# Performance work log

Hardware: AMD Instinct MI355X
Metric: run time of the kernel (lower is better)

Reference implementation:

```python
import jax, jax.numpy as jnp
import numpy as np

NUM_FIELDS = 50
CARD = 10000  # per-field cardinality; global index = x + field_offset
FACTOR_DIM = 64
ATT_SIZE = 64
BATCH = 2048


def setup_inputs() -> dict:
    key = jax.random.key(0)
    ks = jax.random.split(key, 5)
    x = jax.random.randint(ks[0], (BATCH, NUM_FIELDS), 0, CARD, dtype=jnp.int64)
    emb = jax.random.normal(ks[1], (NUM_FIELDS * CARD, FACTOR_DIM), jnp.float32) * 0.1
    W1 = jax.random.normal(ks[2], (FACTOR_DIM, ATT_SIZE), jnp.float32) * 0.1
    b1 = jnp.zeros((ATT_SIZE,), jnp.float32)
    w2 = jax.random.normal(ks[3], (ATT_SIZE, 1), jnp.float32) * 0.1
    b2 = jnp.zeros((1,), jnp.float32)
    lin_w = jax.random.normal(ks[4], (NUM_FIELDS * CARD, 1), jnp.float32) * 0.1
    lin_b = jnp.zeros((1,), jnp.float32)
    return {"x": x, "emb": emb, "W1": W1, "b1": b1, "w2": w2, "b2": b2,
            "lin_w": lin_w, "lin_b": lin_b}


def reference(x, emb, W1, b1, w2, b2, lin_w, lin_b):
    F = NUM_FIELDS
    offsets = (jnp.arange(F, dtype=x.dtype) * CARD)[None, :]  # [1, F]
    idx = x + offsets                                          # [B, F] global ids
    factors = emb[idx]                                         # [B, F, D]
    iu, ju = np.triu_indices(F, k=1)                           # P = F*(F-1)/2 pairs (i < j)
    inter = factors[:, iu, :] * factors[:, ju, :]              # [B, P, D]
    # attention MLP: Dense -> ReLU -> Dense(1) -> Softmax over pair axis
    h = jax.nn.relu(jnp.einsum('bpd,da->bpa', inter, W1) + b1)
    logits = jnp.einsum('bpa,ao->bpo', h, w2) + b2             # [B, P, 1]
    scores = jax.nn.softmax(logits, axis=1)
    inter_sum = jnp.sum(inter, axis=-1, keepdims=True)         # [B, P, 1]
    attended = jnp.sum(inter_sum * scores, axis=1)             # [B, 1]
    linear = jnp.sum(lin_w[idx], axis=1) + lin_b               # [B, 1]
    return linear + attended
```

## Files before the change

kernel.cpp:

```cpp
#include <hip/hip_runtime.h>
#include <hip/hip_bf16.h>

#define NF 50
#define NFP 52
#define NG 13
#define NCARD 10000
#define FD 64
#define NB 2
#define FROW 72
#define FBAT (NFP * FROW)

typedef _Float16 h16x8 __attribute__((ext_vector_type(8)));
typedef float f32x4 __attribute__((ext_vector_type(4)));

__global__ __launch_bounds__(256, 4) void afm_main(
    const int* __restrict__ x,
    const float* __restrict__ emb,
    const float* __restrict__ W1,
    const float* __restrict__ b1,
    const float* __restrict__ w2,
    const float* __restrict__ lin_w,
    const float* __restrict__ lin_b,
    float* __restrict__ out)
{
    __shared__ __align__(16) _Float16 fach[NB * FBAT];
    __shared__ float cmb[4][3];

    const int b0   = blockIdx.x * NB;
    const int tid  = threadIdx.x;
    const int lane = tid & 63;
    const int wid  = tid >> 6;
    const int n16  = lane & 15;
    const int quad = lane >> 4;

    for (int t = tid; t < NB * NFP * 8; t += 256) {
        int rowid = t >> 3, q = t & 7;
        int bb = (rowid >= NFP) ? 1 : 0;
        int f = rowid - bb * NFP;
        h16x8 h = {0, 0, 0, 0, 0, 0, 0, 0};
        if (f < NF) {
            int gid = x[(b0 + bb) * NF + f] + f * NCARD;
            const float* src = emb + (size_t)gid * FD + q * 8;
            float4 v0 = *(const float4*)(src);
            float4 v1 = *(const float4*)(src + 4);
            h[0] = (_Float16)v0.x; h[1] = (_Float16)v0.y;
            h[2] = (_Float16)v0.z; h[3] = (_Float16)v0.w;
            h[4] = (_Float16)v1.x; h[5] = (_Float16)v1.y;
            h[6] = (_Float16)v1.z; h[7] = (_Float16)v1.w;
        }
        *(h16x8*)(fach + (size_t)rowid * FROW + q * 8) = h;
    }

    h16x8 afragW[8];
    #pragma unroll
    for (int mt = 0; mt < 4; ++mt) {
        #pragma unroll
        for (int ks = 0; ks < 2; ++ks) {
            h16x8 v;
            #pragma unroll
            for (int jj = 0; jj < 8; ++jj)
                v[jj] = (_Float16)W1[(ks * 32 + quad * 8 + jj) * 64 + mt * 16 + n16];
            afragW[mt * 2 + ks] = v;
        }
    }
    h16x8 aones = {(_Float16)1, (_Float16)1, (_Float16)1, (_Float16)1,
                   (_Float16)1, (_Float16)1, (_Float16)1, (_Float16)1};
    f32x4 b1v[4], w2v[4];
    #pragma unroll
    for (int mt = 0; mt < 4; ++mt) {
        const float4 bb = *(const float4*)(b1 + mt * 16 + quad * 4);
        const float4 ww = *(const float4*)(w2 + mt * 16 + quad * 4);
        b1v[mt] = (f32x4){bb.x, bb.y, bb.z, bb.w};
        w2v[mt] = (f32x4){ww.x, ww.y, ww.z, ww.w};
    }
    __syncthreads();

    const int mybatch = wid >> 1;
    const _Float16* fb = fach + mybatch * FBAT;
    const int a4 = n16 >> 2, b4 = n16 & 3;
    const int gi_lo = (wid & 1) ? 4 : 0;
    const int gi_hi = (wid & 1) ? NG : 4;

    float m = -1e30f, se = 0.f, sei = 0.f;

    for (int gi = gi_lo; gi < gi_hi; ++gi) {
        const int i = gi * 4 + a4;
        const _Float16* ri = fb + (size_t)i * FROW + quad * 8;
        const h16x8 ri0 = *(const h16x8*)(ri);
        const h16x8 ri1 = *(const h16x8*)(ri + 32);
        for (int gj = gi; gj < NG; ++gj) {
            const int j = gj * 4 + b4;
            const _Float16* rj = fb + (size_t)j * FROW + quad * 8;
            h16x8 pr0 = ri0 * (*(const h16x8*)(rj));
            h16x8 pr1 = ri1 * (*(const h16x8*)(rj + 32));

            f32x4 accS = __builtin_amdgcn_mfma_f32_16x16x32_f16(aones, pr0, (f32x4){0.f, 0.f, 0.f, 0.f}, 0, 0, 0);
            accS = __builtin_amdgcn_mfma_f32_16x16x32_f16(aones, pr1, accS, 0, 0, 0);

            float lacc = 0.f;
            #pragma unroll
            for (int mt = 0; mt < 4; ++mt) {
                f32x4 acc = __builtin_amdgcn_mfma_f32_16x16x32_f16(afragW[mt * 2 + 0], pr0, b1v[mt], 0, 0, 0);
                acc = __builtin_amdgcn_mfma_f32_16x16x32_f16(afragW[mt * 2 + 1], pr1, acc, 0, 0, 0);
                #pragma unroll
                for (int r = 0; r < 4; ++r)
                    lacc += fmaxf(acc[r], 0.f) * w2v[mt][r];
            }
            lacc += __shfl_xor(lacc, 16, 64);
            lacc += __shfl_xor(lacc, 32, 64);

            const bool valid = (i < j) && (j < NF);
            float nm = fmaxf(m, valid ? lacc : -1e30f);
            float sc = __expf(m - nm);
            float e  = valid ? __expf(lacc - nm) : 0.f;
            se  = se * sc + e;
            sei = sei * sc + e * accS[0];
            m = nm;
        }
    }

    #pragma unroll
    for (int d = 1; d <= 8; d <<= 1) {
        float m2   = __shfl_xor(m, d, 64);
        float se2  = __shfl_xor(se, d, 64);
        float sei2 = __shfl_xor(sei, d, 64);
        float nm = fmaxf(m, m2);
        float a = __expf(m - nm), bsc = __expf(m2 - nm);
        se  = se * a + se2 * bsc;
        sei = sei * a + sei2 * bsc;
        m = nm;
    }

    float lin = 0.f;
    if ((wid & 1) == 0) {
        if (lane < NF) {
            int gid = x[(b0 + mybatch) * NF + lane] + lane * NCARD;
            lin = lin_w[gid];
        }
        #pragma unroll
        for (int d = 1; d <= 32; d <<= 1) lin += __shfl_xor(lin, d, 64);
    }

    if (lane == 0) { cmb[wid][0] = m; cmb[wid][1] = se; cmb[wid][2] = sei; }
    __syncthreads();
    if ((wid & 1) == 0 && lane == 0) {
        float m2 = cmb[wid + 1][0], se2 = cmb[wid + 1][1], sei2 = cmb[wid + 1][2];
        float nm = fmaxf(m, m2);
        float a = __expf(m - nm), bsc = __expf(m2 - nm);
        float tse  = se * a + se2 * bsc;
        float tsei = sei * a + sei2 * bsc;
        out[b0 + mybatch] = lin + lin_b[0] + tsei / tse;
    }
}

extern "C" void kernel_launch(void* const* d_in, const int* in_sizes, int n_in,
                              void* d_out, int out_size, void* d_ws, size_t ws_size,
                              hipStream_t stream) {
    const int*   x     = (const int*)d_in[0];
    const float* emb   = (const float*)d_in[1];
    const float* W1    = (const float*)d_in[2];
    const float* b1    = (const float*)d_in[3];
    const float* w2    = (const float*)d_in[4];
    const float* lin_w = (const float*)d_in[6];
    const float* lin_b = (const float*)d_in[7];
    float* out = (float*)d_out;
    const int batch = out_size;
    afm_main<<<batch / NB, 256, 0, stream>>>(x, emb, W1, b1, w2, lin_w, lin_b, out);
}
```

Measured before the change: 217.2 us.

## One batch row per block, pre-pack W1 fragments, drop online-softmax max tracking

```diff
diff --git a/kernel.cpp b/kernel.cpp
--- a/kernel.cpp
+++ b/kernel.cpp
@@ -6,40 +6,53 @@
 #define NG 13
 #define NCARD 10000
 #define FD 64
-#define NB 2
 #define FROW 72
-#define FBAT (NFP * FROW)
 
 typedef _Float16 h16x8 __attribute__((ext_vector_type(8)));
 typedef float f32x4 __attribute__((ext_vector_type(4)));
 
+__global__ void afm_pre(const float* __restrict__ W1, _Float16* __restrict__ w1f) {
+    const int slot = blockIdx.x * 4 + (threadIdx.x >> 6);
+    const int lane = threadIdx.x & 63;
+    const int n16 = lane & 15, quad = lane >> 4;
+    const int mt = slot >> 1, ks = slot & 1;
+    h16x8 v;
+    #pragma unroll
+    for (int jj = 0; jj < 8; ++jj)
+        v[jj] = (_Float16)W1[(ks * 32 + quad * 8 + jj) * 64 + mt * 16 + n16];
+    *(h16x8*)(w1f + ((size_t)(slot * 64 + lane)) * 8) = v;
+}
+
 __global__ __launch_bounds__(256, 4) void afm_main(
     const int* __restrict__ x,
     const float* __restrict__ emb,
-    const float* __restrict__ W1,
     const float* __restrict__ b1,
     const float* __restrict__ w2,
     const float* __restrict__ lin_w,
     const float* __restrict__ lin_b,
+    const _Float16* __restrict__ w1f,
     float* __restrict__ out)
 {
-    __shared__ __align__(16) _Float16 fach[NB * FBAT];
-    __shared__ float cmb[4][3];
+    __shared__ __align__(16) _Float16 fach[NFP * FROW];
+    __shared__ float cmb[4][2];
+    __shared__ float s_lin;
 
-    const int b0   = blockIdx.x * NB;
+    const int b    = blockIdx.x;
     const int tid  = threadIdx.x;
     const int lane = tid & 63;
     const int wid  = tid >> 6;
     const int n16  = lane & 15;
     const int quad = lane >> 4;
 
-    for (int t = tid; t < NB * NFP * 8; t += 256) {
-        int rowid = t >> 3, q = t & 7;
-        int bb = (rowid >= NFP) ? 1 : 0;
-        int f = rowid - bb * NFP;
+    float linv = 0.f;
+    if (wid == 3 && lane < NF)
+        linv = lin_w[x[b * NF + lane] + lane * NCARD];
+
+    for (int t = tid; t < NFP * 8; t += 256) {
+        int f = t >> 3, q = t & 7;
         h16x8 h = {0, 0, 0, 0, 0, 0, 0, 0};
         if (f < NF) {
-            int gid = x[(b0 + bb) * NF + f] + f * NCARD;
+            int gid = x[b * NF + f] + f * NCARD;
             const float* src = emb + (size_t)gid * FD + q * 8;
             float4 v0 = *(const float4*)(src);
             float4 v1 = *(const float4*)(src + 4);
@@ -48,21 +61,13 @@
             h[4] = (_Float16)v1.x; h[5] = (_Float16)v1.y;
             h[6] = (_Float16)v1.z; h[7] = (_Float16)v1.w;
         }
-        *(h16x8*)(fach + (size_t)rowid * FROW + q * 8) = h;
+        *(h16x8*)(fach + (size_t)f * FROW + q * 8) = h;
     }
 
     h16x8 afragW[8];
     #pragma unroll
-    for (int mt = 0; mt < 4; ++mt) {
-        #pragma unroll
-        for (int ks = 0; ks < 2; ++ks) {
-            h16x8 v;
-            #pragma unroll
-            for (int jj = 0; jj < 8; ++jj)
-                v[jj] = (_Float16)W1[(ks * 32 + quad * 8 + jj) * 64 + mt * 16 + n16];
-            afragW[mt * 2 + ks] = v;
-        }
-    }
+    for (int s = 0; s < 8; ++s)
+        afragW[s] = *(const h16x8*)(w1f + ((size_t)(s * 64 + lane)) * 8);
     h16x8 aones = {(_Float16)1, (_Float16)1, (_Float16)1, (_Float16)1,
                    (_Float16)1, (_Float16)1, (_Float16)1, (_Float16)1};
     f32x4 b1v[4], w2v[4];
@@ -75,81 +80,69 @@
     }
     __syncthreads();
 
-    const int mybatch = wid >> 1;
-    const _Float16* fb = fach + mybatch * FBAT;
     const int a4 = n16 >> 2, b4 = n16 & 3;
-    const int gi_lo = (wid & 1) ? 4 : 0;
-    const int gi_hi = (wid & 1) ? NG : 4;
+    float se = 0.f, sei = 0.f;
 
-    float m = -1e30f, se = 0.f, sei = 0.f;
-
-    for (int gi = gi_lo; gi < gi_hi; ++gi) {
+    for (int gi = wid; gi < NG; gi += 4) {
         const int i = gi * 4 + a4;
-        const _Float16* ri = fb + (size_t)i * FROW + quad * 8;
+        const _Float16* ri = fach + (size_t)i * FROW + quad * 8;
         const h16x8 ri0 = *(const h16x8*)(ri);
         const h16x8 ri1 = *(const h16x8*)(ri + 32);
+
+        const _Float16* rjp = fach + (size_t)(gi * 4 + b4) * FROW + quad * 8;
+        h16x8 nj0 = *(const h16x8*)(rjp);
+        h16x8 nj1 = *(const h16x8*)(rjp + 32);
+
         for (int gj = gi; gj < NG; ++gj) {
-            const int j = gj * 4 + b4;
-            const _Float16* rj = fb + (size_t)j * FROW + quad * 8;
-            h16x8 pr0 = ri0 * (*(const h16x8*)(rj));
-            h16x8 pr1 = ri1 * (*(const h16x8*)(rj + 32));
+            h16x8 rj0 = nj0, rj1 = nj1;
+            if (gj + 1 < NG) {
+                rjp += 4 * FROW;
+                nj0 = *(const h16x8*)(rjp);
+                nj1 = *(const h16x8*)(rjp + 32);
+            }
+            h16x8 pr0 = ri0 * rj0;
+            h16x8 pr1 = ri1 * rj1;
 
             f32x4 accS = __builtin_amdgcn_mfma_f32_16x16x32_f16(aones, pr0, (f32x4){0.f, 0.f, 0.f, 0.f}, 0, 0, 0);
             accS = __builtin_amdgcn_mfma_f32_16x16x32_f16(aones, pr1, accS, 0, 0, 0);
 
-            float lacc = 0.f;
+            float lp[4];
             #pragma unroll
             for (int mt = 0; mt < 4; ++mt) {
                 f32x4 acc = __builtin_amdgcn_mfma_f32_16x16x32_f16(afragW[mt * 2 + 0], pr0, b1v[mt], 0, 0, 0);
                 acc = __builtin_amdgcn_mfma_f32_16x16x32_f16(afragW[mt * 2 + 1], pr1, acc, 0, 0, 0);
-                #pragma unroll
-                for (int r = 0; r < 4; ++r)
-                    lacc += fmaxf(acc[r], 0.f) * w2v[mt][r];
+                float s0 = fmaxf(acc[0], 0.f) * w2v[mt][0] + fmaxf(acc[1], 0.f) * w2v[mt][1];
+                float s1 = fmaxf(acc[2], 0.f) * w2v[mt][2] + fmaxf(acc[3], 0.f) * w2v[mt][3];
+                lp[mt] = s0 + s1;
             }
+            float lacc = (lp[0] + lp[1]) + (lp[2] + lp[3]);
             lacc += __shfl_xor(lacc, 16, 64);
             lacc += __shfl_xor(lacc, 32, 64);
 
+            const int j = gj * 4 + b4;
             const bool valid = (i < j) && (j < NF);
-            float nm = fmaxf(m, valid ? lacc : -1e30f);
-            float sc = __expf(m - nm);
-            float e  = valid ? __expf(lacc - nm) : 0.f;
-            se  = se * sc + e;
-            sei = sei * sc + e * accS[0];
-            m = nm;
+            float e = valid ? __expf(lacc) : 0.f;
+            se  += e;
+            sei += e * accS[0];
         }
     }
 
     #pragma unroll
     for (int d = 1; d <= 8; d <<= 1) {
-        float m2   = __shfl_xor(m, d, 64);
-        float se2  = __shfl_xor(se, d, 64);
-        float sei2 = __shfl_xor(sei, d, 64);
-        float nm = fmaxf(m, m2);
-        float a = __expf(m - nm), bsc = __expf(m2 - nm);
-        se  = se * a + se2 * bsc;
-        sei = sei * a + sei2 * bsc;
-        m = nm;
+        se  += __shfl_xor(se, d, 64);
+        sei += __shfl_xor(sei, d, 64);
     }
-
-    float lin = 0.f;
-    if ((wid & 1) == 0) {
-        if (lane < NF) {
-            int gid = x[(b0 + mybatch) * NF + lane] + lane * NCARD;
-            lin = lin_w[gid];
-        }
+    if (wid == 3) {
         #pragma unroll
-        for (int d = 1; d <= 32; d <<= 1) lin += __shfl_xor(lin, d, 64);
+        for (int d = 1; d <= 32; d <<= 1) linv += __shfl_xor(linv, d, 64);
+        if (lane == 0) s_lin = linv;
     }
-
-    if (lane == 0) { cmb[wid][0] = m; cmb[wid][1] = se; cmb[wid][2] = sei; }
+    if (lane == 0) { cmb[wid][0] = se; cmb[wid][1] = sei; }
     __syncthreads();
-    if ((wid & 1) == 0 && lane == 0) {
-        float m2 = cmb[wid + 1][0], se2 = cmb[wid + 1][1], sei2 = cmb[wid + 1][2];
-        float nm = fmaxf(m, m2);
-        float a = __expf(m - nm), bsc = __expf(m2 - nm);
-        float tse  = se * a + se2 * bsc;
-        float tsei = sei * a + sei2 * bsc;
-        out[b0 + mybatch] = lin + lin_b[0] + tsei / tse;
+    if (tid == 0) {
+        float tse  = (cmb[0][0] + cmb[1][0]) + (cmb[2][0] + cmb[3][0]);
+        float tsei = (cmb[0][1] + cmb[1][1]) + (cmb[2][1] + cmb[3][1]);
+        out[b] = s_lin + lin_b[0] + tsei / tse;
     }
 }
 
@@ -164,6 +157,9 @@
     const float* lin_w = (const float*)d_in[6];
     const float* lin_b = (const float*)d_in[7];
     float* out = (float*)d_out;
+
+    _Float16* w1f = (_Float16*)d_ws;
+    afm_pre<<<2, 256, 0, stream>>>(W1, w1f);
     const int batch = out_size;
-    afm_main<<<batch / NB, 256, 0, stream>>>(x, emb, W1, b1, w2, lin_w, lin_b, out);
+    afm_main<<<batch, 256, 0, stream>>>(x, emb, b1, w2, lin_w, lin_b, w1f, out);
 }
```

New measurement: 216.6 us. No clear change (-0.3%).
